# Performance work log

Hardware: AMD Instinct MI355X
Metric: run time of the kernel (lower is better)

Reference implementation:

```python
import jax, jax.numpy as jnp
import numpy as np

B, N, C, H, HD, HH, WW, K, ALPHA = 8, 4096, 256, 8, 32, 64, 64, 5, 4.0


def setup_inputs() -> dict:
    key = jax.random.key(0)
    ks = jax.random.split(key, 6)
    return {
        "x": jax.random.normal(ks[0], (B, N, C), jnp.float32),
        "W_qg": jax.random.normal(ks[1], (C, 2 * C), jnp.float32) * 0.02,
        "W_kv": jax.random.normal(ks[2], (C, 2 * C), jnp.float32) * 0.02,
        "W_proj": jax.random.normal(ks[3], (C, C), jnp.float32) * 0.02,
        "b_proj": jnp.zeros((C,), jnp.float32),
        "dwc_w": jax.random.normal(ks[4], (HD, 1, K, K), jnp.float32) * 0.05,
        "dwc_b": jnp.zeros((HD,), jnp.float32),
        "power_p": jnp.zeros((1, H, 1, HD), jnp.float32),
    }


def _safe_pow(x, p):
    # x >= 0 (post-relu). 0**p == 0 for p > 0; guard base so grads stay finite.
    xs = jnp.where(x > 0, x, 1.0)
    return jnp.where(x > 0, xs ** p, 0.0)


def reference(x, W_qg, W_kv, W_proj, b_proj, dwc_w, dwc_b, power_p):
    qg = x @ W_qg                                  # (B,N,2C)
    q, g = qg[..., :C], qg[..., C:]
    kv = x @ W_kv                                  # (B,N,2C)
    k = kv[..., :C].reshape(B, N, H, HD).transpose(0, 2, 1, 3)   # (B,H,N,hd)
    v = kv[..., C:].reshape(B, N, H, HD).transpose(0, 2, 1, 3)
    q = q.reshape(B, N, H, HD).transpose(0, 2, 1, 3)

    power = 1.0 + ALPHA * jax.nn.sigmoid(power_p)  # (1,H,1,hd)
    # x_s = q_pos@kv_s + q_neg@kv_s = (q_pos+q_neg)@kv_s, kv_s = (k_pos+k_neg)^T v_s
    q_sum = _safe_pow(jax.nn.relu(q), power) + _safe_pow(jax.nn.relu(-q), power)
    k_sum = _safe_pow(jax.nn.relu(k), power) + _safe_pow(jax.nn.relu(-k), power)

    v_s, v_o = v[..., : HD // 2], v[..., HD // 2 :]
    kv_s = jnp.einsum('bhnd,bhne->bhde', k_sum, v_s)
    kv_o = jnp.einsum('bhnd,bhne->bhde', k_sum, v_o)
    x_s = jnp.einsum('bhnd,bhde->bhne', q_sum, kv_s)
    x_o = jnp.einsum('bhnd,bhde->bhne', q_sum, kv_o)
    x_att = jnp.concatenate([x_s, x_o], -1).transpose(0, 2, 1, 3).reshape(B, N, C)

    # depthwise conv branch: exact layout replication of torch permute/reshape chain
    v_img = v.transpose(0, 2, 1, 3).reshape(B * H, HD, HH, WW)
    pad = K // 2
    v_loc = jax.lax.conv_general_dilated(
        v_img, dwc_w, (1, 1), [(pad, pad), (pad, pad)],
        feature_group_count=HD,
        dimension_numbers=('NCHW', 'OIHW', 'NCHW')) + dwc_b[None, :, None, None]
    v_loc = v_loc.reshape(B, H, HD, N).transpose(0, 2, 1, 3).reshape(B, C, N).transpose(0, 2, 1)

    return ((x_att + v_loc) * g) @ W_proj + b_proj
```

## Files before the change

kernel.cpp:

```cpp
#include <hip/hip_runtime.h>
#include <hip/hip_bf16.h>
#include <math.h>

#define B_ 8
#define N_ 4096
#define C_ 256
#define H_ 8
#define HD_ 32
#define BN_ (B_ * N_)
#define E_ ((size_t)BN_ * C_)

typedef __attribute__((ext_vector_type(8))) short short8;
typedef __attribute__((ext_vector_type(4))) float f32x4;

__device__ __forceinline__ float b2f(__hip_bfloat16 x) { return __bfloat162float(x); }

__device__ __forceinline__ void gl_lds16(const void* gp, void* lp) {
    __builtin_amdgcn_global_load_lds(
        (const __attribute__((address_space(1))) unsigned int*)gp,
        (__attribute__((address_space(3))) unsigned int*)lp,
        16, 0, 0);
}

__device__ __forceinline__ float fast_abspow(float v, float p) {
    float av = fabsf(v);
    return (av > 0.f) ? __builtin_amdgcn_exp2f(p * __builtin_amdgcn_logf(av)) : 0.f;
}

__device__ __forceinline__ float bf_lo(unsigned u) { return __uint_as_float(u << 16); }
__device__ __forceinline__ float bf_hi(unsigned u) { return __uint_as_float(u & 0xffff0000u); }
__device__ __forceinline__ unsigned short f2bfbits(float f) {
    __hip_bfloat16 h = __float2bfloat16(f);
    return *(unsigned short*)&h;
}
__device__ __forceinline__ unsigned pack2(float lo, float hi) {
    return (unsigned)f2bfbits(lo) | ((unsigned)f2bfbits(hi) << 16);
}

__global__ __launch_bounds__(256) void cvt_all(
    const float* __restrict__ x, const float* __restrict__ Wqg,
    const float* __restrict__ Wkv, const float* __restrict__ Wp,
    const float* __restrict__ pp,
    __hip_bfloat16* __restrict__ xb, __hip_bfloat16* __restrict__ Wt1,
    __hip_bfloat16* __restrict__ Wt2, float* __restrict__ powers,
    float* __restrict__ kv_mat2)
{
    int t = threadIdx.x;
    int bid0 = blockIdx.x;
    if (bid0 < 4096) {
        size_t i = ((size_t)bid0 * 256 + t) * 8;
        float4 a = *(const float4*)&x[i];
        float4 b = *(const float4*)&x[i + 4];
        uint4 o = {pack2(a.x, a.y), pack2(a.z, a.w), pack2(b.x, b.y), pack2(b.z, b.w)};
        *(uint4*)&xb[i] = o;
        return;
    }
    int bid = bid0 - 4096;
    if (bid == 80) {
        powers[t] = 1.0f + 4.0f / (1.0f + expf(-pp[t]));
        return;
    }
    if (bid >= 81) {
        ((float4*)kv_mat2)[(size_t)(bid - 81) * 256 + t] = (float4){0.f, 0.f, 0.f, 0.f};
        return;
    }
    __shared__ float tile[64][65];
    const float* src;
    __hip_bfloat16* dst;
    int scols, tr, tc, dn0;
    if (bid < 32)      { src = Wqg; scols = 512; tr = bid >> 3;        tc = bid & 7;        dst = Wt1; dn0 = tc * 64; }
    else if (bid < 64) { src = Wkv; scols = 512; tr = (bid - 32) >> 3; tc = (bid - 32) & 7; dst = Wt1; dn0 = 512 + tc * 64; }
    else               { src = Wp;  scols = 256; tr = (bid - 64) >> 2; tc = (bid - 64) & 3; dst = Wt2; dn0 = tc * 64; }
    int tx = t & 63, ty = t >> 6;
    #pragma unroll
    for (int i = 0; i < 16; i++) {
        int r = ty + i * 4;
        tile[r][tx] = src[(size_t)(tr * 64 + r) * scols + tc * 64 + tx];
    }
    __syncthreads();
    #pragma unroll
    for (int i = 0; i < 16; i++) {
        int n_local = ty + i * 4;
        dst[(size_t)(dn0 + n_local) * 256 + tr * 64 + tx] = __float2bfloat16(tile[tx][n_local]);
    }
}

__global__ __launch_bounds__(256) void gemm1_mfma(
    const __hip_bfloat16* __restrict__ xb, const __hip_bfloat16* __restrict__ Wt1,
    const float* __restrict__ powers,
    __hip_bfloat16* __restrict__ q16, __hip_bfloat16* __restrict__ k16,
    __hip_bfloat16* __restrict__ g16, __hip_bfloat16* __restrict__ v16)
{
    __shared__ __align__(16) unsigned short As[2 * 128 * 32];
    __shared__ __align__(16) unsigned short Bs[2 * 128 * 32];
    int t = threadIdx.x;
    int w = t >> 6, l = t & 63;
    int bswz = (blockIdx.x & 7) * 256 + (blockIdx.x >> 3);
    int row0 = (bswz >> 3) * 128;
    int colb = bswz & 7;
    int col0 = colb * 128;
    int wm = (w >> 1) * 64, wn = (w & 1) * 64;
    int lane15 = l & 15, quad = l >> 4;
    int srow = l >> 2;
    int skcol = (l & 3) * 8;

    f32x4 acc[4][4];
    #pragma unroll
    for (int mi = 0; mi < 4; mi++)
        #pragma unroll
        for (int ni = 0; ni < 4; ni++) acc[mi][ni] = (f32x4){0.f, 0.f, 0.f, 0.f};

    for (int k0 = 0; k0 < 256; k0 += 64) {
        #pragma unroll
        for (int kh = 0; kh < 2; kh++) {
            #pragma unroll
            for (int i = 0; i < 2; i++) {
                int r = i * 64 + w * 16 + srow;
                int kc = k0 + kh * 32 + skcol;
                gl_lds16(&xb[(size_t)(row0 + r) * 256 + kc],
                         &As[kh * 4096 + (i * 64 + w * 16) * 32]);
                gl_lds16(&Wt1[(size_t)(col0 + r) * 256 + kc],
                         &Bs[kh * 4096 + (i * 64 + w * 16) * 32]);
            }
        }
        __syncthreads();
        #pragma unroll
        for (int kh = 0; kh < 2; kh++) {
            short8 a[4], b[4];
            #pragma unroll
            for (int mi = 0; mi < 4; mi++)
                a[mi] = *(const short8*)&As[kh * 4096 + (wm + mi * 16 + lane15) * 32 + quad * 8];
            #pragma unroll
            for (int ni = 0; ni < 4; ni++)
                b[ni] = *(const short8*)&Bs[kh * 4096 + (wn + ni * 16 + lane15) * 32 + quad * 8];
            #pragma unroll
            for (int mi = 0; mi < 4; mi++)
                #pragma unroll
                for (int ni = 0; ni < 4; ni++)
                    acc[mi][ni] = __builtin_amdgcn_mfma_f32_16x16x32_bf16(a[mi], b[ni], acc[mi][ni], 0, 0, 0);
        }
        __syncthreads();
    }

    int region = colb >> 1;
    bool dopow = (region == 0) || (region == 2);
    __hip_bfloat16* dst = (region == 0) ? q16 : (region == 1) ? g16 : (region == 2) ? k16 : v16;
    #pragma unroll
    for (int mi = 0; mi < 4; mi++) {
        #pragma unroll
        for (int ni = 0; ni < 4; ni++) {
            int row = row0 + wm + mi * 16 + quad * 4;
            int col = col0 + wn + ni * 16 + lane15;
            int c255 = col & 255;
            float p = powers[c255];
            #pragma unroll
            for (int r = 0; r < 4; r++) {
                float v = acc[mi][ni][r];
                float o = dopow ? fast_abspow(v, p) : v;
                dst[(size_t)(row + r) * 256 + c255] = __float2bfloat16(o);
            }
        }
    }
}

__global__ __launch_bounds__(256) void kvmat_kernel(
    const __hip_bfloat16* __restrict__ k16, const __hip_bfloat16* __restrict__ v16,
    float* __restrict__ kv_mat2)
{
    __shared__ __align__(16) unsigned short Kl[16 * 256];
    __shared__ __align__(16) unsigned short Vl[16 * 256];
    int t = threadIdx.x;
    int bid = blockIdx.x;
    int b = bid >> 6, seg = bid & 63;
    int h = t >> 5;
    float acc[32];
    #pragma unroll
    for (int e = 0; e < 32; e++) acc[e] = 0.f;
    const size_t base = (size_t)b * N_ * 256;
    int row = t >> 4, colb = (t & 15) * 16;
    for (int n0 = seg * 64; n0 < seg * 64 + 64; n0 += 16) {
        const uint4* ks = (const uint4*)(k16 + base + (size_t)(n0 + row) * 256 + colb);
        uint4 ka = ks[0], kb = ks[1];
        const uint4* vs = (const uint4*)(v16 + base + (size_t)(n0 + row) * 256 + colb);
        uint4 va = vs[0], vb = vs[1];
        __syncthreads();
        uint4* kd4 = (uint4*)&Kl[row * 256 + colb];
        kd4[0] = ka; kd4[1] = kb;
        uint4* vd4 = (uint4*)&Vl[row * 256 + colb];
        vd4[0] = va; vd4[1] = vb;
        __syncthreads();
        #pragma unroll
        for (int nn = 0; nn < 16; nn++) {
            float kd = bf_lo((unsigned)Kl[nn * 256 + t]);
            const uint4* vp = (const uint4*)&Vl[nn * 256 + h * 32];
            uint4 v0 = vp[0], v1 = vp[1], v2 = vp[2], v3 = vp[3];
            unsigned us[16] = {v0.x, v0.y, v0.z, v0.w, v1.x, v1.y, v1.z, v1.w,
                               v2.x, v2.y, v2.z, v2.w, v3.x, v3.y, v3.z, v3.w};
            #pragma unroll
            for (int j = 0; j < 16; j++) {
                acc[2 * j]     += kd * bf_lo(us[j]);
                acc[2 * j + 1] += kd * bf_hi(us[j]);
            }
        }
    }
    float* dst = kv_mat2 + (size_t)b * 8192;
    #pragma unroll
    for (int e = 0; e < 32; e++) atomicAdd(&dst[e * 256 + t], acc[e]);
}

__global__ __launch_bounds__(256) void conv_kernel(
    const __hip_bfloat16* __restrict__ v16,
    const float* __restrict__ w, const float* __restrict__ bias,
    __hip_bfloat16* __restrict__ vloc)
{
    __shared__ __align__(16) float img[64 * 72];
    __shared__ float wl[25];
    int t = threadIdx.x;
    int gid = blockIdx.x;
    int DD = gid & 31;
    if (t < 128) {
        int row = t >> 1, side = (t & 1) * 68;
        *(float4*)&img[row * 72 + side] = (float4){0.f, 0.f, 0.f, 0.f};
    }
    if (t < 25) wl[t] = w[DD * 25 + t];
    {
        int row = t >> 2, colb = (t & 3) * 16;
        const uint4* src = (const uint4*)(v16 + (size_t)gid * 4096 + row * 64 + colb);
        uint4 u0 = src[0], u1 = src[1];
        float4* d = (float4*)&img[row * 72 + 4 + colb];
        d[0] = (float4){bf_lo(u0.x), bf_hi(u0.x), bf_lo(u0.y), bf_hi(u0.y)};
        d[1] = (float4){bf_lo(u0.z), bf_hi(u0.z), bf_lo(u0.w), bf_hi(u0.w)};
        d[2] = (float4){bf_lo(u1.x), bf_hi(u1.x), bf_lo(u1.y), bf_hi(u1.y)};
        d[3] = (float4){bf_lo(u1.z), bf_hi(u1.z), bf_lo(u1.w), bf_hi(u1.w)};
    }
    __syncthreads();
    float bs = bias[DD];
    int x0 = (t & 15) * 4, yb = t >> 4;
    #pragma unroll
    for (int s = 0; s < 4; s++) {
        int y = yb + s * 16;
        float a0 = bs, a1 = bs, a2 = bs, a3 = bs;
        #pragma unroll
        for (int ky = 0; ky < 5; ky++) {
            int row = y + ky - 2;
            if (row < 0 || row >= 64) continue;
            const float* rp = &img[row * 72 + x0];
            float4 w0 = *(const float4*)rp;
            float4 w1 = *(const float4*)(rp + 4);
            float4 w2 = *(const float4*)(rp + 8);
            float win[12] = {w0.x, w0.y, w0.z, w0.w, w1.x, w1.y, w1.z, w1.w,
                             w2.x, w2.y, w2.z, w2.w};
            #pragma unroll
            for (int kx = 0; kx < 5; kx++) {
                float wt = wl[ky * 5 + kx];
                a0 += wt * win[2 + kx];
                a1 += wt * win[3 + kx];
                a2 += wt * win[4 + kx];
                a3 += wt * win[5 + kx];
            }
        }
        unsigned lo = pack2(a0, a1);
        unsigned hi = pack2(a2, a3);
        *(uint2*)(vloc + (size_t)gid * 4096 + y * 64 + x0) = (uint2){lo, hi};
    }
}

#define A2P 264
__global__ __launch_bounds__(256) void att_gemm2(
    const __hip_bfloat16* __restrict__ q16, const float* __restrict__ kv_mat2,
    const __hip_bfloat16* __restrict__ vloc, const __hip_bfloat16* __restrict__ g16,
    const __hip_bfloat16* __restrict__ Wt2, const float* __restrict__ bp,
    float* __restrict__ out)
{
    __shared__ __align__(16) unsigned short QA[64 * A2P];
    __shared__ __align__(16) unsigned short Bs[2 * 256 * 32];
    int t = threadIdx.x;
    int w = t >> 6, l = t & 63;
    int r0 = blockIdx.x * 64;
    int b = r0 >> 12, n0 = r0 & 4095;
    int lane15 = l & 15, quad = l >> 4;
    int h0 = w * 2;

    {
        const uint4* qsrc = (const uint4*)(q16 + (size_t)(r0 + (t >> 2)) * 256 + (t & 3) * 64);
        uint4* qdst = (uint4*)&QA[(t >> 2) * A2P + (t & 3) * 64];
        #pragma unroll
        for (int j = 0; j < 8; j++) qdst[j] = qsrc[j];
    }
    __syncthreads();

    short8 afr[4][2];
    #pragma unroll
    for (int m = 0; m < 4; m++)
        #pragma unroll
        for (int hh = 0; hh < 2; hh++)
            afr[m][hh] = *(const short8*)&QA[(m * 16 + lane15) * A2P + (h0 + hh) * 32 + quad * 8];

    short8 bfr[2][2];
    #pragma unroll
    for (int hh = 0; hh < 2; hh++) {
        #pragma unroll
        for (int nt = 0; nt < 2; nt++) {
            const float4* kp = (const float4*)(kv_mat2 + (size_t)b * 8192 +
                (size_t)(nt * 16 + lane15) * 256 + (h0 + hh) * 32 + quad * 8);
            float4 ka = kp[0], kb = kp[1];
            short8 bb;
            bb[0] = (short)f2bfbits(ka.x); bb[1] = (short)f2bfbits(ka.y);
            bb[2] = (short)f2bfbits(ka.z); bb[3] = (short)f2bfbits(ka.w);
            bb[4] = (short)f2bfbits(kb.x); bb[5] = (short)f2bfbits(kb.y);
            bb[6] = (short)f2bfbits(kb.z); bb[7] = (short)f2bfbits(kb.w);
            bfr[hh][nt] = bb;
        }
    }

    f32x4 ac[4][2][2];
    #pragma unroll
    for (int m = 0; m < 4; m++)
        #pragma unroll
        for (int hh = 0; hh < 2; hh++)
            #pragma unroll
            for (int nt = 0; nt < 2; nt++)
                ac[m][hh][nt] = __builtin_amdgcn_mfma_f32_16x16x32_bf16(
                    afr[m][hh], bfr[hh][nt], (f32x4){0.f, 0.f, 0.f, 0.f}, 0, 0, 0);

    #pragma unroll
    for (int m = 0; m < 4; m++) {
        #pragma unroll
        for (int hh = 0; hh < 2; hh++) {
            #pragma unroll
            for (int nt = 0; nt < 2; nt++) {
                int col = (h0 + hh) * 32 + nt * 16 + lane15;
                int rowb = m * 16 + quad * 4;
                size_t img = ((size_t)((b * 8 + (col & 7)) * 32 + (col >> 3))) * 4096 + n0 + rowb;
                uint2 vv = *(const uint2*)(vloc + img);
                float vl[4] = {bf_lo(vv.x), bf_hi(vv.x), bf_lo(vv.y), bf_hi(vv.y)};
                #pragma unroll
                for (int i = 0; i < 4; i++) {
                    float gg = b2f(g16[(size_t)(r0 + rowb + i) * 256 + col]);
                    float val = (ac[m][hh][nt][i] + vl[i]) * gg;
                    QA[(rowb + i) * A2P + col] = f2bfbits(val);
                }
            }
        }
    }

    int wm = (w & 1) * 32, wn = (w >> 1) * 128;
    f32x4 acc2[2][8];
    #pragma unroll
    for (int mi = 0; mi < 2; mi++)
        #pragma unroll
        for (int ni = 0; ni < 8; ni++) acc2[mi][ni] = (f32x4){0.f, 0.f, 0.f, 0.f};

    for (int k0 = 0; k0 < 256; k0 += 64) {
        __syncthreads();
        #pragma unroll
        for (int h2 = 0; h2 < 2; h2++) {
            #pragma unroll
            for (int i = 0; i < 4; i++) {
                int ncol = i * 64 + w * 16 + (l >> 2);
                gl_lds16(&Wt2[(size_t)ncol * 256 + k0 + h2 * 32 + (l & 3) * 8],
                         &Bs[h2 * 8192 + (i * 64 + w * 16) * 32]);
            }
        }
        __syncthreads();
        #pragma unroll
        for (int h2 = 0; h2 < 2; h2++) {
            short8 a[2], bb[8];
            #pragma unroll
            for (int mi = 0; mi < 2; mi++)
                a[mi] = *(const short8*)&QA[(wm + mi * 16 + lane15) * A2P + k0 + h2 * 32 + quad * 8];
            #pragma unroll
            for (int ni = 0; ni < 8; ni++)
                bb[ni] = *(const short8*)&Bs[h2 * 8192 + (wn + ni * 16 + lane15) * 32 + quad * 8];
            #pragma unroll
            for (int mi = 0; mi < 2; mi++)
                #pragma unroll
                for (int ni = 0; ni < 8; ni++)
                    acc2[mi][ni] = __builtin_amdgcn_mfma_f32_16x16x32_bf16(a[mi], bb[ni], acc2[mi][ni], 0, 0, 0);
        }
    }

    #pragma unroll
    for (int mi = 0; mi < 2; mi++) {
        #pragma unroll
        for (int ni = 0; ni < 8; ni++) {
            int row = r0 + wm + mi * 16 + quad * 4;
            int col = wn + ni * 16 + lane15;
            float bv = bp[col];
            #pragma unroll
            for (int r = 0; r < 4; r++)
                out[(size_t)(row + r) * 256 + col] = acc2[mi][ni][r] + bv;
        }
    }
}

extern "C" void kernel_launch(void* const* d_in, const int* in_sizes, int n_in,
                              void* d_out, int out_size, void* d_ws, size_t ws_size,
                              hipStream_t stream) {
    const float* x      = (const float*)d_in[0];
    const float* W_qg   = (const float*)d_in[1];
    const float* W_kv   = (const float*)d_in[2];
    const float* W_proj = (const float*)d_in[3];
    const float* b_proj = (const float*)d_in[4];
    const float* dwc_w  = (const float*)d_in[5];
    const float* dwc_b  = (const float*)d_in[6];
    const float* pow_p  = (const float*)d_in[7];
    float* out = (float*)d_out;

    float* ws = (float*)d_ws;
    const size_t E = E_;
    __hip_bfloat16* q16  = (__hip_bfloat16*)ws;
    __hip_bfloat16* k16  = (__hip_bfloat16*)(ws + E / 2);
    __hip_bfloat16* g16  = (__hip_bfloat16*)(ws + E);
    __hip_bfloat16* v16  = (__hip_bfloat16*)(ws + 3 * E / 2);
    __hip_bfloat16* xb   = (__hip_bfloat16*)(ws + 2 * E);
    __hip_bfloat16* vl16 = (__hip_bfloat16*)(ws + 5 * E / 2);
    float* kv_mat2 = ws + 3 * E;
    __hip_bfloat16* Wt1 = (__hip_bfloat16*)(kv_mat2 + 65536);
    __hip_bfloat16* Wt2 = Wt1 + 262144;
    float* powers = (float*)(Wt2 + 65536);

    cvt_all<<<4096 + 81 + 64, 256, 0, stream>>>(x, W_qg, W_kv, W_proj, pow_p, xb, Wt1, Wt2, powers, kv_mat2);
    gemm1_mfma<<<2048, 256, 0, stream>>>(xb, Wt1, powers, q16, k16, g16, v16);
    kvmat_kernel<<<512, 256, 0, stream>>>(k16, v16, kv_mat2);
    conv_kernel<<<2048, 256, 0, stream>>>(v16, dwc_w, dwc_b, vl16);
    att_gemm2<<<512, 256, 0, stream>>>(q16, kv_mat2, vl16, g16, Wt2, b_proj, out);
}
```

Baseline: 204.4 us.

## Compute per-head K^T V with MFMA instead of scalar FMA loops

Replaces the scalar-FMA kvmat kernel with an MFMA-based one. Each block handles one (batch, head) pair over a 512-token segment, stages K and V transposed into LDS, and runs bf16 16x16x32 MFMAs. The four waves' partial results are reduced in LDS before atomics. This cuts ALU work and the number of atomics, at the cost of strided 2-byte transposing LDS stores that may bank-conflict.

```diff
diff --git a/kernel.cpp b/kernel.cpp
--- a/kernel.cpp
+++ b/kernel.cpp
@@ -163,49 +163,80 @@
     }
 }
 
-__global__ __launch_bounds__(256) void kvmat_kernel(
+__global__ __launch_bounds__(256) void kvmat_mfma(
     const __hip_bfloat16* __restrict__ k16, const __hip_bfloat16* __restrict__ v16,
     float* __restrict__ kv_mat2)
 {
-    __shared__ __align__(16) unsigned short Kl[16 * 256];
-    __shared__ __align__(16) unsigned short Vl[16 * 256];
+    __shared__ __align__(16) unsigned short KV[2][32][136];
     int t = threadIdx.x;
+    int w = t >> 6, l = t & 63;
+    int lane15 = l & 15, quad = l >> 4;
     int bid = blockIdx.x;
-    int b = bid >> 6, seg = bid & 63;
-    int h = t >> 5;
-    float acc[32];
-    #pragma unroll
-    for (int e = 0; e < 32; e++) acc[e] = 0.f;
-    const size_t base = (size_t)b * N_ * 256;
-    int row = t >> 4, colb = (t & 15) * 16;
-    for (int n0 = seg * 64; n0 < seg * 64 + 64; n0 += 16) {
-        const uint4* ks = (const uint4*)(k16 + base + (size_t)(n0 + row) * 256 + colb);
-        uint4 ka = ks[0], kb = ks[1];
-        const uint4* vs = (const uint4*)(v16 + base + (size_t)(n0 + row) * 256 + colb);
-        uint4 va = vs[0], vb = vs[1];
-        __syncthreads();
-        uint4* kd4 = (uint4*)&Kl[row * 256 + colb];
-        kd4[0] = ka; kd4[1] = kb;
-        uint4* vd4 = (uint4*)&Vl[row * 256 + colb];
-        vd4[0] = va; vd4[1] = vb;
-        __syncthreads();
-        #pragma unroll
-        for (int nn = 0; nn < 16; nn++) {
-            float kd = bf_lo((unsigned)Kl[nn * 256 + t]);
-            const uint4* vp = (const uint4*)&Vl[nn * 256 + h * 32];
-            uint4 v0 = vp[0], v1 = vp[1], v2 = vp[2], v3 = vp[3];
-            unsigned us[16] = {v0.x, v0.y, v0.z, v0.w, v1.x, v1.y, v1.z, v1.w,
-                               v2.x, v2.y, v2.z, v2.w, v3.x, v3.y, v3.z, v3.w};
-            #pragma unroll
-            for (int j = 0; j < 16; j++) {
-                acc[2 * j]     += kd * bf_lo(us[j]);
-                acc[2 * j + 1] += kd * bf_hi(us[j]);
-            }
-        }
-    }
-    float* dst = kv_mat2 + (size_t)b * 8192;
-    #pragma unroll
-    for (int e = 0; e < 32; e++) atomicAdd(&dst[e * 256 + t], acc[e]);
+    int pair = bid >> 3, seg = bid & 7;
+    int b = pair >> 3, h = pair & 7;
+    int nloc = t & 127, cs = (t >> 7) * 16;
+
+    f32x4 acc[2][2];
+    #pragma unroll
+    for (int di = 0; di < 2; di++)
+        #pragma unroll
+        for (int ei = 0; ei < 2; ei++) acc[di][ei] = (f32x4){0.f, 0.f, 0.f, 0.f};
+
+    const size_t base = (size_t)b * N_ * 256 + h * 32 + cs;
+    for (int c4 = 0; c4 < 4; c4++) {
+        int n0 = seg * 512 + c4 * 128;
+        const uint4* kp = (const uint4*)(k16 + base + (size_t)(n0 + nloc) * 256);
+        uint4 ka = kp[0], kb = kp[1];
+        const uint4* vp = (const uint4*)(v16 + base + (size_t)(n0 + nloc) * 256);
+        uint4 va = vp[0], vb = vp[1];
+        __syncthreads();
+        unsigned kw[8] = {ka.x, ka.y, ka.z, ka.w, kb.x, kb.y, kb.z, kb.w};
+        unsigned vw[8] = {va.x, va.y, va.z, va.w, vb.x, vb.y, vb.z, vb.w};
+        #pragma unroll
+        for (int j = 0; j < 8; j++) {
+            KV[0][cs + 2 * j][nloc]     = (unsigned short)(kw[j] & 0xffffu);
+            KV[0][cs + 2 * j + 1][nloc] = (unsigned short)(kw[j] >> 16);
+            KV[1][cs + 2 * j][nloc]     = (unsigned short)(vw[j] & 0xffffu);
+            KV[1][cs + 2 * j + 1][nloc] = (unsigned short)(vw[j] >> 16);
+        }
+        __syncthreads();
+        int nb = w * 32 + quad * 8;
+        short8 a[2], bb[2];
+        #pragma unroll
+        for (int di = 0; di < 2; di++)
+            a[di] = *(const short8*)&KV[0][di * 16 + lane15][nb];
+        #pragma unroll
+        for (int ei = 0; ei < 2; ei++)
+            bb[ei] = *(const short8*)&KV[1][ei * 16 + lane15][nb];
+        #pragma unroll
+        for (int di = 0; di < 2; di++)
+            #pragma unroll
+            for (int ei = 0; ei < 2; ei++)
+                acc[di][ei] = __builtin_amdgcn_mfma_f32_16x16x32_bf16(a[di], bb[ei], acc[di][ei], 0, 0, 0);
+    }
+
+    __syncthreads();
+    float* red = (float*)KV;
+    #pragma unroll
+    for (int di = 0; di < 2; di++)
+        #pragma unroll
+        for (int ei = 0; ei < 2; ei++) {
+            int e = ei * 16 + lane15;
+            #pragma unroll
+            for (int r = 0; r < 4; r++) {
+                int d = di * 16 + quad * 4 + r;
+                red[w * 1056 + e * 33 + d] = acc[di][ei][r];
+            }
+        }
+    __syncthreads();
+    #pragma unroll
+    for (int j = 0; j < 4; j++) {
+        int o = j * 256 + t;
+        int e = o >> 5, d = o & 31;
+        float s = red[e * 33 + d] + red[1056 + e * 33 + d]
+                + red[2112 + e * 33 + d] + red[3168 + e * 33 + d];
+        atomicAdd(&kv_mat2[(size_t)b * 8192 + e * 256 + h * 32 + d], s);
+    }
 }
 
 __global__ __launch_bounds__(256) void conv_kernel(
@@ -422,7 +453,7 @@
 
     cvt_all<<<4096 + 81 + 64, 256, 0, stream>>>(x, W_qg, W_kv, W_proj, pow_p, xb, Wt1, Wt2, powers, kv_mat2);
     gemm1_mfma<<<2048, 256, 0, stream>>>(xb, Wt1, powers, q16, k16, g16, v16);
-    kvmat_kernel<<<512, 256, 0, stream>>>(k16, v16, kv_mat2);
+    kvmat_mfma<<<512, 256, 0, stream>>>(k16, v16, kv_mat2);
     conv_kernel<<<2048, 256, 0, stream>>>(v16, dwc_w, dwc_b, vl16);
     att_gemm2<<<512, 256, 0, stream>>>(q16, kv_mat2, vl16, g16, Wt2, b_proj, out);
 }
```

Result: faster. 175.1 us (-14.3%).
